# Kernel tuning notes

Hardware: AMD Instinct MI355X
Metric: run time of the kernel (lower is better)

The kernel has to match this reference:

```python
import jax, jax.numpy as jnp
import numpy as np

DN = ('NCH', 'OIH', 'NCH')

def conv1d(x, w, b, stride, pad):
    y = jax.lax.conv_general_dilated(x, w, (stride,), [(pad, pad)], dimension_numbers=DN)
    return y + b[None, :, None]

def deconv1d(x, w, b):
    # ConvTranspose1d(k=3, stride=2, padding=1, output_padding=1): L -> 2L
    # expressed as lhs-dilated conv with padding (k-1-p, k-1-p+output_padding) = (1, 2)
    y = jax.lax.conv_general_dilated(x, w, (1,), [(1, 2)], lhs_dilation=(2,), dimension_numbers=DN)
    return y + b[None, :, None]

def setup_inputs() -> dict:
    key = jax.random.key(0)
    ks = jax.random.split(key, 24)
    B, T, A = 256, 512, 32
    H = 256              # hidden_dim / embedding_dim
    K = 8192             # n_embeddings
    enc_ch = [64, 128, 256]
    dec_ch = [256, 128, 64]
    s = 0.05
    inp = {'x': jax.random.normal(ks[0], (B, T, A), jnp.float32)}
    # encoder convs (OIH layout), k=3
    in_ch = A
    for i, ch in enumerate(enc_ch):
        inp[f'enc_w{i}'] = jax.random.normal(ks[1 + 2 * i], (ch, in_ch, 3), jnp.float32) * s
        inp[f'enc_b{i}'] = jnp.zeros((ch,), jnp.float32)
        in_ch = ch
    inp['proj_w'] = jax.random.normal(ks[8], (H, enc_ch[-1], 1), jnp.float32) * s
    inp['proj_b'] = jnp.zeros((H,), jnp.float32)
    inp['embedding'] = jax.random.normal(ks[9], (K, H), jnp.float32)
    # decoder deconvs (stored directly in conv OIH form)
    in_ch = H
    for i, ch in enumerate(dec_ch + [A]):
        inp[f'dec_w{i}'] = jax.random.normal(ks[10 + 2 * i], (ch, in_ch, 3), jnp.float32) * s
        inp[f'dec_b{i}'] = jnp.zeros((ch,), jnp.float32)
        in_ch = ch
    return inp

def _forward(x, enc_w0, enc_b0, enc_w1, enc_b1, enc_w2, enc_b2, proj_w, proj_b,
             embedding, dec_w0, dec_b0, dec_w1, dec_b1, dec_w2, dec_b2, dec_w3, dec_b3):
    # ---- encoder ----
    h = jnp.transpose(x, (0, 2, 1))                      # (B, A, T)
    h = jax.nn.relu(conv1d(h, enc_w0, enc_b0, 2, 1))
    h = jax.nn.relu(conv1d(h, enc_w1, enc_b1, 2, 1))
    h = jax.nn.relu(conv1d(h, enc_w2, enc_b2, 2, 1))
    z_e = conv1d(h, proj_w, proj_b, 1, 0)                # (B, H, T/8)
    # ---- EMA vector quantizer (eval-mode math) ----
    B, C, T = z_e.shape
    flat = jnp.transpose(z_e, (0, 2, 1)).reshape(-1, C)  # (B*T, C)
    dist = (jnp.sum(flat * flat, axis=1, keepdims=True)
            - 2.0 * flat @ embedding.T
            + jnp.sum(embedding * embedding, axis=1))    # (B*T, K)
    indices = jnp.argmin(dist, axis=1)                   # (B*T,)
    z_q = embedding[indices].reshape(B, T, C).transpose(0, 2, 1)  # (B, C, T)
    commitment_loss = jnp.mean((jax.lax.stop_gradient(z_e) - z_q) ** 2)
    codebook_loss = jnp.mean((z_e - jax.lax.stop_gradient(z_q)) ** 2)
    z_q = z_e + jax.lax.stop_gradient(z_q - z_e)         # straight-through
    # ---- decoder ----
    d = jax.nn.relu(deconv1d(z_q, dec_w0, dec_b0))
    d = jax.nn.relu(deconv1d(d, dec_w1, dec_b1))
    d = jax.nn.relu(deconv1d(d, dec_w2, dec_b2))
    d = deconv1d(d, dec_w3, dec_b3)                      # (B, A, seq_len)
    out = jnp.transpose(d, (0, 2, 1))                    # (B, seq_len, A)
    return out, codebook_loss, commitment_loss, indices.reshape(B, T)

def reference(x, enc_w0, enc_b0, enc_w1, enc_b1, enc_w2, enc_b2, proj_w, proj_b,
              embedding, dec_w0, dec_b0, dec_w1, dec_b1, dec_w2, dec_b2, dec_w3, dec_b3):
    return _forward(x, enc_w0, enc_b0, enc_w1, enc_b1, enc_w2, enc_b2, proj_w, proj_b,
                    embedding, dec_w0, dec_b0, dec_w1, dec_b1, dec_w2, dec_b2, dec_w3, dec_b3)
```

## Files before the change

### kernel.cpp

```cpp
#include <hip/hip_runtime.h>


typedef _Float16 half8 __attribute__((ext_vector_type(8)));
typedef _Float16 half4v __attribute__((ext_vector_type(4)));
typedef float f32x4 __attribute__((ext_vector_type(4)));
typedef float f32x16 __attribute__((ext_vector_type(16)));

#define GL_LDS(src, dst) \
  __builtin_amdgcn_global_load_lds((const __attribute__((address_space(1))) void*)(src), \
                                   (__attribute__((address_space(3))) void*)(dst), 16, 0, 0)

struct CP2 {
  const _Float16* inH; const _Float16* inL;
  const _Float16* wH; const _Float16* wL;
  const float* bias; const _Float16* zpad;
  float* outF; _Float16* outH; _Float16* outL;
  const int* vidx;
  int Ci, lg2Ci, Ti, Co, To, K2, stride, pad, lg2U, Umask;
};

template<int SP, int PAR, bool GATHER, bool RELU, int OM>
__global__ __launch_bounds__(256, 4) void conv_mfma(CP2 p) {
  __shared__ _Float16 As[2][SP * 2048];
  __shared__ _Float16 Bs[2][SP * 2048];
  const int tid = threadIdx.x;
  const int w = tid >> 6;
  const int lane = tid & 63;
  const int m = lane & 15, q = lane >> 4;
  const int btbase = blockIdx.x * 64;
  const int cobase = blockIdx.y * 64;
  const int bt = btbase + w * 16 + m;
  const int b = bt >> p.lg2U, u = bt & p.Umask;
  const int nkb = p.K2 >> 5;
  const int lw = w * 512;

  int er0 = 0, er1 = 0;
  if (GATHER) {
    er0 = p.vidx[b * p.Ti + u];
    if (PAR == 1) er1 = (u + 1 < p.Ti) ? p.vidx[b * p.Ti + u + 1] : 0;
  }

  auto stage = [&](int kb, int buf) {
    const int k0 = kb << 5;
    const int tap = k0 >> p.lg2Ci;
    const int ci0 = k0 & (p.Ci - 1);
    int dt;
    if (PAR == 0)      dt = 0;
    else if (PAR == 1) dt = tap;
    else               dt = tap - p.pad;
    const int tin = (PAR < 0) ? u * p.stride + dt : u + dt;
    const bool ok = (tin >= 0) && (tin < p.Ti);
    int ai;
    if (GATHER) {
      const int er = (PAR == 1 && tap == 1) ? er1 : er0;
      ai = er * 256 + ci0 + q * 8;
    } else {
      ai = (b * p.Ti + tin) * p.Ci + ci0 + q * 8;
    }
    GL_LDS(ok ? &p.inH[ai] : p.zpad, &As[buf][lw]);
    if (SP == 2) GL_LDS(ok ? &p.inL[ai] : p.zpad, &As[buf][2048 + lw]);
    const int wb = (blockIdx.y * nkb + kb) * 2048 + lw + lane * 8;
    GL_LDS(&p.wH[wb], &Bs[buf][lw]);
    if (SP == 2) GL_LDS(&p.wL[wb], &Bs[buf][2048 + lw]);
  };

  f32x4 acc[4];
#pragma unroll
  for (int j = 0; j < 4; ++j) acc[j] = {0.f, 0.f, 0.f, 0.f};

  stage(0, 0);
  for (int kb = 0; kb < nkb; ++kb) {
    const int buf = kb & 1;
    __syncthreads();
    if (kb + 1 < nkb) stage(kb + 1, buf ^ 1);
    const half8 a1 = *(const half8*)&As[buf][lw + lane * 8];
    half8 a2;
    if (SP == 2) a2 = *(const half8*)&As[buf][2048 + lw + lane * 8];
#pragma unroll
    for (int ct = 0; ct < 4; ++ct) {
      const half8 b1 = *(const half8*)&Bs[buf][ct * 512 + lane * 8];
      half8 b2;
      if (SP == 2) b2 = *(const half8*)&Bs[buf][2048 + ct * 512 + lane * 8];
      acc[ct] = __builtin_amdgcn_mfma_f32_16x16x32_f16(a1, b1, acc[ct], 0, 0, 0);
      if (SP == 2) {
        acc[ct] = __builtin_amdgcn_mfma_f32_16x16x32_f16(a2, b1, acc[ct], 0, 0, 0);
        acc[ct] = __builtin_amdgcn_mfma_f32_16x16x32_f16(a1, b2, acc[ct], 0, 0, 0);
      }
    }
  }
#pragma unroll
  for (int ct = 0; ct < 4; ++ct) {
    const int co = cobase + ct * 16 + m;
    if (co < p.Co) {
      const float bv = p.bias[co];
#pragma unroll
      for (int j = 0; j < 4; ++j) {
        const int row = btbase + w * 16 + q * 4 + j;
        const int bb = row >> p.lg2U, uu = row & p.Umask;
        float v = acc[ct][j] + bv;
        if (RELU) v = fmaxf(v, 0.f);
        const int t = (PAR < 0) ? uu : 2 * uu + PAR;
        const int oi = (bb * p.To + t) * p.Co + co;
        if (OM == 3) {
          p.outF[oi] = v;
        } else if (OM == 1) {
          p.outH[oi] = (_Float16)v;
        } else {
          const _Float16 h = (_Float16)v;
          const _Float16 l = (_Float16)(v - (float)h);
          p.outH[oi] = h; p.outL[oi] = l;
        }
      }
    }
  }
}

struct CPD {
  const _Float16* inH; const _Float16* wS; const float* bias;
  const _Float16* zpad;
  float* outF; _Float16* outH;
  int Ci, Ti, Co, To, lg2U, Umask;
};

template<bool RELU, bool F32OUT>
__global__ __launch_bounds__(256, 4) void conv_dec(CPD p) {
  __shared__ _Float16 As[2][2560];
  __shared__ _Float16 Bs[2][6144];
  const int tid = threadIdx.x;
  const int w = tid >> 6;
  const int lane = tid & 63;
  const int m = lane & 15, q = lane >> 4;
  const int btbase = blockIdx.x * 64;
  const int cobase = blockIdx.y * 64;
  const int b0 = btbase >> p.lg2U;
  const int u0 = btbase & p.Umask;
  const int nkb = p.Ci >> 5;
  const int lw = w * 512;

  auto stage = [&](int kb, int buf) {
    const int ci0 = kb << 5;
    {
      const int ur = u0 + w * 16 + m;
      const bool ok = ur < p.Ti;
      GL_LDS(ok ? &p.inH[(b0 * p.Ti + ur) * p.Ci + ci0 + q * 8] : p.zpad,
             &As[buf][lw]);
    }
    if (w == 0) {
      const int ur = u0 + 64 + m;
      const bool ok = ur < p.Ti;
      GL_LDS(ok ? &p.inH[(b0 * p.Ti + ur) * p.Ci + ci0 + q * 8] : p.zpad,
             &As[buf][2048]);
    }
    const int wb = (blockIdx.y * nkb + kb) * 6144;
#pragma unroll
    for (int tap = 0; tap < 3; ++tap)
      GL_LDS(&p.wS[wb + tap * 2048 + lw + lane * 8], &Bs[buf][tap * 2048 + lw]);
  };

  f32x4 aE[4], aO[4];
#pragma unroll
  for (int j = 0; j < 4; ++j) { aE[j] = {0.f,0.f,0.f,0.f}; aO[j] = {0.f,0.f,0.f,0.f}; }

  stage(0, 0);
  for (int kb = 0; kb < nkb; ++kb) {
    const int buf = kb & 1;
    __syncthreads();
    if (kb + 1 < nkb) stage(kb + 1, buf ^ 1);
    const int row = w * 16 + m;
    const half8 a0 = *(const half8*)&As[buf][lw + lane * 8];
    const int r1 = row + 1;
    const int s1 = (r1 >> 4) * 512 + ((r1 & 15) + (q << 4)) * 8;
    const half8 a1s = *(const half8*)&As[buf][s1];
#pragma unroll
    for (int ct = 0; ct < 4; ++ct) {
      const half8 w0 = *(const half8*)&Bs[buf][ct * 512 + lane * 8];
      const half8 w1 = *(const half8*)&Bs[buf][2048 + ct * 512 + lane * 8];
      const half8 w2 = *(const half8*)&Bs[buf][4096 + ct * 512 + lane * 8];
      aE[ct] = __builtin_amdgcn_mfma_f32_16x16x32_f16(a0,  w1, aE[ct], 0, 0, 0);
      aO[ct] = __builtin_amdgcn_mfma_f32_16x16x32_f16(a0,  w0, aO[ct], 0, 0, 0);
      aO[ct] = __builtin_amdgcn_mfma_f32_16x16x32_f16(a1s, w2, aO[ct], 0, 0, 0);
    }
  }
#pragma unroll
  for (int ct = 0; ct < 4; ++ct) {
    const int co = cobase + ct * 16 + m;
    if (co < p.Co) {
      const float bv = p.bias[co];
#pragma unroll
      for (int j = 0; j < 4; ++j) {
        const int u = u0 + w * 16 + q * 4 + j;
        float vE = aE[ct][j] + bv;
        float vO = aO[ct][j] + bv;
        if (RELU) { vE = fmaxf(vE, 0.f); vO = fmaxf(vO, 0.f); }
        const int oiE = (b0 * p.To + 2 * u) * p.Co + co;
        const int oiO = oiE + p.Co;
        if (F32OUT) { p.outF[oiE] = vE; p.outF[oiO] = vO; }
        else        { p.outH[oiE] = (_Float16)vE; p.outH[oiO] = (_Float16)vO; }
      }
    }
  }
}


__global__ __launch_bounds__(256) void x_prep(const float* __restrict__ x,
                                              _Float16* __restrict__ h,
                                              _Float16* __restrict__ l,
                                              _Float16* __restrict__ zp) {
  if (blockIdx.x == 0 && threadIdx.x < 64) {
    const uint4 z = {0u, 0u, 0u, 0u};
    ((uint4*)zp)[threadIdx.x] = z;
  }
  const int i = blockIdx.x * 256 + threadIdx.x;
  const float4 v = ((const float4*)x)[i];
  half4v a, b;
  a.x = (_Float16)v.x; b.x = (_Float16)(v.x - (float)a.x);
  a.y = (_Float16)v.y; b.y = (_Float16)(v.y - (float)a.y);
  a.z = (_Float16)v.z; b.z = (_Float16)(v.z - (float)a.z);
  a.w = (_Float16)v.w; b.w = (_Float16)(v.w - (float)a.w);
  ((half4v*)h)[i] = a;
  ((half4v*)l)[i] = b;
}

struct WPE { const float* w; int dh, dl, Ci, lg2Ci, KWO, Co, PAR, SP, nkb, base, dec; };
struct WPA { WPE e[9]; };

__global__ __launch_bounds__(256) void w_prep(WPA a, _Float16* __restrict__ wst) {
  const int b = (int)blockIdx.x;
  int i = 0;
#pragma unroll
  for (int j = 1; j < 9; ++j) if (b >= a.e[j].base) i = j;
  const WPE E = a.e[i];
  const int local = b - E.base;
  const int cb = local / E.nkb;
  const int kb = local - cb * E.nkb;
  const int tid = threadIdx.x;
  const int cc = tid >> 2, g = tid & 3;
  const int co = cb * 64 + cc;
  const bool okc = co < E.Co;
  const int k0 = kb << 5;
  const int tap0 = k0 >> E.lg2Ci;
  const int ci0 = k0 & (E.Ci - 1);
  const int slot = (cc >> 4) * 512 + ((cc & 15) + (g << 4)) * 8;
  if (!E.dec) {
    const int ko = (E.PAR == 0) ? 1 : (E.PAR == 1 ? 2 * tap0 : tap0);
    half8 hv, lv;
#pragma unroll
    for (int j = 0; j < 8; ++j) {
      const float wv = okc ? E.w[(co * E.Ci + ci0 + g * 8 + j) * E.KWO + ko] : 0.f;
      hv[j] = (_Float16)wv;
      lv[j] = (_Float16)(wv - (float)hv[j]);
    }
    const int off = (cb * E.nkb + kb) * 2048 + slot;
    *(half8*)&wst[E.dh + off] = hv;
    if (E.SP == 2) *(half8*)&wst[E.dl + off] = lv;
  } else {
#pragma unroll
    for (int tap = 0; tap < 3; ++tap) {
      half8 hv;
#pragma unroll
      for (int j = 0; j < 8; ++j) {
        const float wv = okc ? E.w[(co * E.Ci + ci0 + g * 8 + j) * 3 + tap] : 0.f;
        hv[j] = (_Float16)wv;
      }
      *(half8*)&wst[E.dh + ((cb * E.nkb + kb) * 3 + tap) * 2048 + slot] = hv;
    }
  }
}

__global__ __launch_bounds__(256) void emb_prep(const float* __restrict__ emb,
                                                _Float16* __restrict__ hi,
                                                _Float16* __restrict__ lo,
                                                float* __restrict__ nrm) {
  const int k = blockIdx.x * 4 + (threadIdx.x >> 6);
  const int lane = threadIdx.x & 63;
  const int i = k * 64 + lane;
  const float4 v = ((const float4*)emb)[i];
  half4v a, b;
  a.x = (_Float16)v.x; b.x = (_Float16)(v.x - (float)a.x);
  a.y = (_Float16)v.y; b.y = (_Float16)(v.y - (float)a.y);
  a.z = (_Float16)v.z; b.z = (_Float16)(v.z - (float)a.z);
  a.w = (_Float16)v.w; b.w = (_Float16)(v.w - (float)a.w);
  ((half4v*)hi)[i] = a;
  ((half4v*)lo)[i] = b;
  double s = (double)v.x * v.x + (double)v.y * v.y +
             (double)v.z * v.z + (double)v.w * v.w;
  for (int off = 32; off; off >>= 1) s += __shfl_down(s, off);
  if (lane == 0) nrm[k] = (float)s;
}

__global__ __launch_bounds__(256, 2) void vq_mfma(const _Float16* __restrict__ z1g,
                                                  const _Float16* __restrict__ z2g,
                                                  const _Float16* __restrict__ e1g,
                                                  const _Float16* __restrict__ e2g,
                                                  const float* __restrict__ nrm,
                                                  float* __restrict__ pbest,
                                                  int* __restrict__ pidx) {
  __shared__ _Float16 es[2 * 2 * 4096];
  const int tid = threadIdx.x;
  const int lane = tid & 63;
  const int w = tid >> 6;
  const int m32 = lane & 31;
  const int hi = lane >> 5;
  const int seg = blockIdx.x & 7, rb = blockIdx.x >> 3;
  const int rbase = rb * 128;
  const int row_g = rbase + w * 32 + m32;

  half8 za[16], zb[16];
#pragma unroll
  for (int c = 0; c < 16; ++c) {
    const int zi = row_g * 256 + c * 16 + hi * 8;
    za[c] = *(const half8*)&z1g[zi];
    zb[c] = *(const half8*)&z2g[zi];
  }

  float best[16]; int bk[16];
#pragma unroll
  for (int i = 0; i < 16; ++i) { best[i] = 3.4e38f; bk[i] = 0; }

  const int sbase = (seg * 1024 + ((tid >> 7) & 1) * 32 + (tid & 31)) * 256
                  + ((tid >> 6) & 1) * 16 + ((tid >> 5) & 1) * 8;
  const int lw = w * 512;

  auto stage = [&](int cc_, int kb_, int buf_) {
    const int off = sbase + cc_ * 32768 + kb_ * 32;
    __builtin_amdgcn_global_load_lds(
        (const __attribute__((address_space(1))) void*)(e1g + off),
        (__attribute__((address_space(3))) void*)&es[(buf_ * 2 + 0) * 4096 + lw], 16, 0, 0);
    __builtin_amdgcn_global_load_lds(
        (const __attribute__((address_space(1))) void*)(e1g + off + 16384),
        (__attribute__((address_space(3))) void*)&es[(buf_ * 2 + 0) * 4096 + 2048 + lw], 16, 0, 0);
    __builtin_amdgcn_global_load_lds(
        (const __attribute__((address_space(1))) void*)(e2g + off),
        (__attribute__((address_space(3))) void*)&es[(buf_ * 2 + 1) * 4096 + lw], 16, 0, 0);
    __builtin_amdgcn_global_load_lds(
        (const __attribute__((address_space(1))) void*)(e2g + off + 16384),
        (__attribute__((address_space(3))) void*)&es[(buf_ * 2 + 1) * 4096 + 2048 + lw], 16, 0, 0);
  };

  stage(0, 0, 0);

  const int lb = lane * 8;
  f32x16 acc[4];
  for (int cc = 0; cc < 8; ++cc) {
    const int cbase = seg * 1024 + cc * 128;
#pragma unroll
    for (int ct = 0; ct < 4; ++ct) {
#pragma unroll
      for (int rg = 0; rg < 16; ++rg) acc[ct][rg] = 0.f;
    }
#pragma unroll
    for (int kb = 0; kb < 8; ++kb) {
      const int buf = kb & 1;
      const _Float16* e1s = &es[(buf * 2 + 0) * 4096];
      const _Float16* e2s = &es[(buf * 2 + 1) * 4096];
      __syncthreads();
      if (kb < 7)      stage(cc, kb + 1, buf ^ 1);
      else if (cc < 7) stage(cc + 1, 0, buf ^ 1);
      __builtin_amdgcn_s_setprio(1);
#pragma unroll
      for (int ct = 0; ct < 4; ++ct) {
#pragma unroll
        for (int k16 = 0; k16 < 2; ++k16) {
          const half8 b1 = *(const half8*)&e1s[ct * 1024 + k16 * 512 + lb];
          const half8 b2 = *(const half8*)&e2s[ct * 1024 + k16 * 512 + lb];
          const half8 a1 = za[kb * 2 + k16];
          const half8 a2 = zb[kb * 2 + k16];
          acc[ct] = __builtin_amdgcn_mfma_f32_32x32x16_f16(a1, b1, acc[ct], 0, 0, 0);
          acc[ct] = __builtin_amdgcn_mfma_f32_32x32x16_f16(a2, b1, acc[ct], 0, 0, 0);
          acc[ct] = __builtin_amdgcn_mfma_f32_32x32x16_f16(a1, b2, acc[ct], 0, 0, 0);
        }
      }
      __builtin_amdgcn_s_setprio(0);
    }
#pragma unroll
    for (int ct = 0; ct < 4; ++ct) {
      const int k = cbase + ct * 32 + m32;
      const float nv = nrm[k];
#pragma unroll
      for (int rg = 0; rg < 16; ++rg) {
        const float d = nv - 2.f * acc[ct][rg];
        if (d < best[rg]) { best[rg] = d; bk[rg] = k; }
      }
    }
  }
#pragma unroll
  for (int rg = 0; rg < 16; ++rg) {
    float bv = best[rg]; int kv = bk[rg];
    for (int off = 1; off < 32; off <<= 1) {
      const float ob = __shfl_xor(bv, off);
      const int ok = __shfl_xor(kv, off);
      if (ob < bv || (ob == bv && ok < kv)) { bv = ob; kv = ok; }
    }
    if (m32 == 0) {
      const int row = rbase + w * 32 + (rg & 3) + 8 * (rg >> 2) + 4 * hi;
      pbest[seg * 16384 + row] = bv;
      pidx[seg * 16384 + row] = kv;
    }
  }
}

__global__ void merge_kernel(const float* __restrict__ pbest, const int* __restrict__ pidx,
                             int* __restrict__ vidx, float* __restrict__ out_idx,
                             float* __restrict__ lacc) {
  const int n = blockIdx.x * 256 + threadIdx.x;
  float bv = pbest[n]; int kv = pidx[n];
#pragma unroll
  for (int s = 1; s < 8; ++s) {
    const float ob = pbest[s * 16384 + n];
    const int ok = pidx[s * 16384 + n];
    if (ob < bv || (ob == bv && ok < kv)) { bv = ob; kv = ok; }
  }
  vidx[n] = kv;
  out_idx[n] = (float)kv;
  if (n == 0) *lacc = 0.f;
}

__global__ __launch_bounds__(256) void loss_kernel(const _Float16* __restrict__ z1g,
                                                   const _Float16* __restrict__ z2g,
                                                   const float* __restrict__ emb,
                                                   const int* __restrict__ vidx,
                                                   float* __restrict__ lacc) {
  const int g4 = blockIdx.x * 256 + threadIdx.x;
  const int e0 = g4 * 4;
  const int n = e0 >> 8, c = e0 & 255;
  const half4v a = ((const half4v*)z1g)[g4];
  const half4v b = ((const half4v*)z2g)[g4];
  const float4 q4 = *(const float4*)&emb[vidx[n] * 256 + c];
  const float dx = ((float)a.x + (float)b.x) - q4.x;
  const float dy = ((float)a.y + (float)b.y) - q4.y;
  const float dz = ((float)a.z + (float)b.z) - q4.z;
  const float dw = ((float)a.w + (float)b.w) - q4.w;
  float s = dx * dx + dy * dy + dz * dz + dw * dw;
  for (int off = 32; off; off >>= 1) s += __shfl_down(s, off);
  __shared__ float red[4];
  if ((threadIdx.x & 63) == 0) red[threadIdx.x >> 6] = s;
  __syncthreads();
  if (threadIdx.x == 0) atomicAdd(lacc, red[0] + red[1] + red[2] + red[3]);
}

__global__ void fin_kernel(const float* __restrict__ lacc, float* __restrict__ out, int loff) {
  if (threadIdx.x == 0) {
    const float l = *lacc * (1.f / 4194304.f);
    out[loff] = l;
    out[loff + 1] = l;
  }
}

extern "C" void kernel_launch(void* const* d_in, const int* in_sizes, int n_in,
                              void* d_out, int out_size, void* d_ws, size_t ws_size,
                              hipStream_t stream) {
  const float* x   = (const float*)d_in[0];
  const float* ew0 = (const float*)d_in[1];  const float* eb0 = (const float*)d_in[2];
  const float* ew1 = (const float*)d_in[3];  const float* eb1 = (const float*)d_in[4];
  const float* ew2 = (const float*)d_in[5];  const float* eb2 = (const float*)d_in[6];
  const float* pw  = (const float*)d_in[7];  const float* pb  = (const float*)d_in[8];
  const float* emb = (const float*)d_in[9];
  const float* dw0 = (const float*)d_in[10]; const float* db0 = (const float*)d_in[11];
  const float* dw1 = (const float*)d_in[12]; const float* db1 = (const float*)d_in[13];
  const float* dw2 = (const float*)d_in[14]; const float* db2 = (const float*)d_in[15];
  const float* dw3 = (const float*)d_in[16]; const float* db3 = (const float*)d_in[17];
  float* ws  = (float*)d_ws;
  float* out = (float*)d_out;

  const int A0 = 0, B0 = 4194304, C0 = 8388608, TL = 12582912;
  _Float16* h0h = (_Float16*)(ws + C0);
  _Float16* h0l = h0h + 4194304;
  _Float16* h1h = (_Float16*)(ws + B0);
  _Float16* h1l = h1h + 4194304;
  _Float16* h2h = (_Float16*)(ws + A0);
  _Float16* h2l = h2h + 4194304;
  _Float16* h3h = (_Float16*)(ws + B0);
  _Float16* h3l = h3h + 4194304;
  _Float16* z1g = (_Float16*)(ws + A0);
  _Float16* z2g = z1g + 4194304;
  _Float16* e1g = (_Float16*)(ws + B0);
  _Float16* e2g = e1g + 2097152;
  float* pbest = ws + B0 + 2097152;
  int*   pidx  = (int*)(ws + B0 + 2097152 + 131072);
  _Float16* d1h = (_Float16*)(ws + C0);
  _Float16* d2h = (_Float16*)(ws + A0);
  _Float16* d3h = (_Float16*)(ws + B0);
  float* nrm  = ws + TL;
  int*   vidx = (int*)(ws + TL + 8192);
  float* lacc = ws + TL + 8192 + 16384;
  _Float16* zpad = (_Float16*)(ws + TL + 26624);
  _Float16* wst = (_Float16*)(ws + TL + 32768);

  const int W_E0H = 0,      W_E0L = 6144;
  const int W_E1H = 12288,  W_E1L = 36864;
  const int W_E2H = 61440,  W_E2L = 159744;
  const int W_PJH = 258048, W_PJL = 323584;
  const int W_D0A = 389120, W_D0B = 454656;
  const int W_DC1 = 585728, W_DC2 = 684032, W_DC3 = 708608;

  const int idx_off  = out_size - 16384;
  const int loss_off = out_size - 16386;

  x_prep<<<4096, 256, 0, stream>>>(x, h0h, h0l, zpad);
  WPA wa;
  wa.e[0] = {ew0, W_E0H, W_E0L, 32,  5, 3, 64,  -1, 2, 3,  0,   0};
  wa.e[1] = {ew1, W_E1H, W_E1L, 64,  6, 3, 128, -1, 2, 6,  3,   0};
  wa.e[2] = {ew2, W_E2H, W_E2L, 128, 7, 3, 256, -1, 2, 12, 15,  0};
  wa.e[3] = {pw,  W_PJH, W_PJL, 256, 8, 1, 256, -1, 2, 8,  63,  0};
  wa.e[4] = {dw0, W_D0A, 0,     256, 8, 3, 256,  0, 1, 8,  95,  0};
  wa.e[5] = {dw0, W_D0B, 0,     256, 8, 3, 256,  1, 1, 16, 127, 0};
  wa.e[6] = {dw1, W_DC1, 0,     256, 8, 3, 128, -1, 1, 8,  191, 1};
  wa.e[7] = {dw2, W_DC2, 0,     128, 7, 3, 64,  -1, 1, 4,  207, 1};
  wa.e[8] = {dw3, W_DC3, 0,     64,  6, 3, 32,  -1, 1, 2,  211, 1};
  w_prep<<<213, 256, 0, stream>>>(wa, wst);

  CP2 p; p.vidx = nullptr; p.inH = nullptr; p.inL = nullptr;
  p.outF = nullptr; p.outH = nullptr; p.outL = nullptr; p.zpad = zpad;

  p.inH = h0h; p.inL = h0l; p.wH = wst + W_E0H; p.wL = wst + W_E0L;
  p.bias = eb0; p.outH = h1h; p.outL = h1l;
  p.Ci = 32; p.lg2Ci = 5; p.Ti = 512; p.Co = 64; p.To = 256;
  p.K2 = 96; p.stride = 2; p.pad = 1; p.lg2U = 8; p.Umask = 255;
  conv_mfma<2, -1, false, true, 0><<<dim3(1024, 1), 256, 0, stream>>>(p);

  p.inH = h1h; p.inL = h1l; p.wH = wst + W_E1H; p.wL = wst + W_E1L;
  p.bias = eb1; p.outH = h2h; p.outL = h2l;
  p.Ci = 64; p.lg2Ci = 6; p.Ti = 256; p.Co = 128; p.To = 128; p.K2 = 192;
  p.lg2U = 7; p.Umask = 127;
  conv_mfma<2, -1, false, true, 0><<<dim3(512, 2), 256, 0, stream>>>(p);

  p.inH = h2h; p.inL = h2l; p.wH = wst + W_E2H; p.wL = wst + W_E2L;
  p.bias = eb2; p.outH = h3h; p.outL = h3l;
  p.Ci = 128; p.lg2Ci = 7; p.Ti = 128; p.Co = 256; p.To = 64; p.K2 = 384;
  p.lg2U = 6; p.Umask = 63;
  conv_mfma<2, -1, false, true, 0><<<dim3(256, 4), 256, 0, stream>>>(p);

  p.inH = h3h; p.inL = h3l; p.wH = wst + W_PJH; p.wL = wst + W_PJL;
  p.bias = pb; p.outH = z1g; p.outL = z2g;
  p.Ci = 256; p.lg2Ci = 8; p.Ti = 64; p.Co = 256; p.To = 64;
  p.K2 = 256; p.stride = 1; p.pad = 0; p.lg2U = 6; p.Umask = 63;
  conv_mfma<2, -1, false, false, 0><<<dim3(256, 4), 256, 0, stream>>>(p);

  emb_prep<<<2048, 256, 0, stream>>>(emb, e1g, e2g, nrm);
  vq_mfma<<<1024, 256, 0, stream>>>(z1g, z2g, e1g, e2g, nrm, pbest, pidx);
  merge_kernel<<<64, 256, 0, stream>>>(pbest, pidx, vidx, out + idx_off, lacc);
  loss_kernel<<<4096, 256, 0, stream>>>(z1g, z2g, emb, vidx, lacc);
  fin_kernel<<<1, 64, 0, stream>>>(lacc, out, loss_off);

  p.inH = e1g; p.inL = nullptr; p.bias = db0;
  p.outH = d1h; p.outL = nullptr; p.vidx = vidx;
  p.Ci = 256; p.lg2Ci = 8; p.Ti = 64; p.Co = 256; p.To = 128;
  p.lg2U = 6; p.Umask = 63;
  p.wH = wst + W_D0A; p.wL = nullptr;
  p.K2 = 256; conv_mfma<1, 0, true, true, 1><<<dim3(256, 4), 256, 0, stream>>>(p);
  p.wH = wst + W_D0B;
  p.K2 = 512; conv_mfma<1, 1, true, true, 1><<<dim3(256, 4), 256, 0, stream>>>(p);

  CPD d; d.zpad = zpad;
  d.inH = d1h; d.wS = wst + W_DC1; d.bias = db1; d.outF = nullptr; d.outH = d2h;
  d.Ci = 256; d.Ti = 128; d.Co = 128; d.To = 256; d.lg2U = 7; d.Umask = 127;
  conv_dec<true, false><<<dim3(512, 2), 256, 0, stream>>>(d);

  d.inH = d2h; d.wS = wst + W_DC2; d.bias = db2; d.outH = d3h;
  d.Ci = 128; d.Ti = 256; d.Co = 64; d.To = 512; d.lg2U = 8; d.Umask = 255;
  conv_dec<true, false><<<dim3(1024, 1), 256, 0, stream>>>(d);

  d.inH = d3h; d.wS = wst + W_DC3; d.bias = db3; d.outF = out; d.outH = nullptr;
  d.Ci = 64; d.Ti = 512; d.Co = 32; d.To = 1024; d.lg2U = 9; d.Umask = 511;
  conv_dec<false, true><<<dim3(2048, 1), 256, 0, stream>>>(d);
}
```

Before: 498.4 us.

## Triple-buffer LDS staging with partial vmcnt waits in conv kernels

Both the encoder/VQ conv kernel and the decoder transposed-conv kernel move from double to triple buffering of the LDS tiles. Two k-blocks are prefetched ahead, and a partial s_waitcnt vmcnt replaces the full __syncthreads drain, so global-to-LDS loads for the next tile can stay in flight during the MFMAs. The aim is to hide global load latency. In exchange, LDS use grows by half, which may lower occupancy, and the hand-counted vmcnt values must exactly match the number of loads each wave issues per stage.

Result: slower. 514.8 us (+3.3%).

```diff
diff --git a/kernel.cpp b/kernel.cpp
--- a/kernel.cpp
+++ b/kernel.cpp
@@ -21,8 +21,8 @@
 
 template<int SP, int PAR, bool GATHER, bool RELU, int OM>
 __global__ __launch_bounds__(256, 4) void conv_mfma(CP2 p) {
-  __shared__ _Float16 As[2][SP * 2048];
-  __shared__ _Float16 Bs[2][SP * 2048];
+  __shared__ _Float16 As[3][SP * 2048];
+  __shared__ _Float16 Bs[3][SP * 2048];
   const int tid = threadIdx.x;
   const int w = tid >> 6;
   const int lane = tid & 63;
@@ -69,10 +69,21 @@
   for (int j = 0; j < 4; ++j) acc[j] = {0.f, 0.f, 0.f, 0.f};
 
   stage(0, 0);
+  stage(1, 1);
+  int buf = 0;
   for (int kb = 0; kb < nkb; ++kb) {
-    const int buf = kb & 1;
-    __syncthreads();
-    if (kb + 1 < nkb) stage(kb + 1, buf ^ 1);
+    if (kb + 1 < nkb) {
+      if (SP == 2) asm volatile("s_waitcnt vmcnt(4)" ::: "memory");
+      else         asm volatile("s_waitcnt vmcnt(2)" ::: "memory");
+    } else {
+      asm volatile("s_waitcnt vmcnt(0)" ::: "memory");
+    }
+    __builtin_amdgcn_s_barrier();
+    __builtin_amdgcn_sched_barrier(0);
+    if (kb + 2 < nkb) {
+      const int b2 = (buf + 2 >= 3) ? buf - 1 : buf + 2;
+      stage(kb + 2, b2);
+    }
     const half8 a1 = *(const half8*)&As[buf][lw + lane * 8];
     half8 a2;
     if (SP == 2) a2 = *(const half8*)&As[buf][2048 + lw + lane * 8];
@@ -87,6 +98,7 @@
         acc[ct] = __builtin_amdgcn_mfma_f32_16x16x32_f16(a1, b2, acc[ct], 0, 0, 0);
       }
     }
+    buf = (buf + 1 == 3) ? 0 : buf + 1;
   }
 #pragma unroll
   for (int ct = 0; ct < 4; ++ct) {
@@ -124,8 +136,8 @@
 
 template<bool RELU, bool F32OUT>
 __global__ __launch_bounds__(256, 4) void conv_dec(CPD p) {
-  __shared__ _Float16 As[2][2560];
-  __shared__ _Float16 Bs[2][6144];
+  __shared__ _Float16 As[3][2560];
+  __shared__ _Float16 Bs[3][6144];
   const int tid = threadIdx.x;
   const int w = tid >> 6;
   const int lane = tid & 63;
@@ -162,10 +174,21 @@
   for (int j = 0; j < 4; ++j) { aE[j] = {0.f,0.f,0.f,0.f}; aO[j] = {0.f,0.f,0.f,0.f}; }
 
   stage(0, 0);
+  stage(1, 1);
+  int buf = 0;
   for (int kb = 0; kb < nkb; ++kb) {
-    const int buf = kb & 1;
-    __syncthreads();
-    if (kb + 1 < nkb) stage(kb + 1, buf ^ 1);
+    if (kb + 1 < nkb) {
+      if (w == 0) asm volatile("s_waitcnt vmcnt(5)" ::: "memory");
+      else        asm volatile("s_waitcnt vmcnt(4)" ::: "memory");
+    } else {
+      asm volatile("s_waitcnt vmcnt(0)" ::: "memory");
+    }
+    __builtin_amdgcn_s_barrier();
+    __builtin_amdgcn_sched_barrier(0);
+    if (kb + 2 < nkb) {
+      const int b2 = (buf + 2 >= 3) ? buf - 1 : buf + 2;
+      stage(kb + 2, b2);
+    }
     const int row = w * 16 + m;
     const half8 a0 = *(const half8*)&As[buf][lw + lane * 8];
     const int r1 = row + 1;
@@ -180,6 +203,7 @@
       aO[ct] = __builtin_amdgcn_mfma_f32_16x16x32_f16(a0,  w0, aO[ct], 0, 0, 0);
       aO[ct] = __builtin_amdgcn_mfma_f32_16x16x32_f16(a1s, w2, aO[ct], 0, 0, 0);
     }
+    buf = (buf + 1 == 3) ? 0 : buf + 1;
   }
 #pragma unroll
   for (int ct = 0; ct < 4; ++ct) {
```
